# Performance work log

Hardware: AMD Instinct MI355X
Metric: run time of the kernel (lower is better)

Reference implementation:

```python
import jax, jax.numpy as jnp
import numpy as np

N = 40000            # atoms
ER = 2_500_000       # radial edges
EA = 1_200_000       # angular edges
P = 4_000_000        # angle triples
NUM_SPECIES = 4      # H,C,N,O
CUTOFF = 5.2
ANG_CUTOFF = 3.5
RADIAL_ETA = 16.0
ANGULAR_ETA = 8.0
RDIV = 16
ADIV = 4
ZETA = 32.0
ASEC = 4
RSTART = 0.8
ASTART = 0.8


def setup_inputs() -> dict:
    key = jax.random.key(0)
    ks = jax.random.split(key, 12)
    species = jax.random.randint(ks[0], (N,), 0, NUM_SPECIES, dtype=jnp.int32)
    rad_distances = jax.random.uniform(ks[1], (ER,), jnp.float32, RSTART, CUTOFF)
    rad_switch = jax.random.uniform(ks[2], (ER,), jnp.float32)
    edge_src = jax.random.randint(ks[3], (ER,), 0, N, dtype=jnp.int32)
    edge_dst = jax.random.randint(ks[4], (ER,), 0, N, dtype=jnp.int32)
    ang_distances = jax.random.uniform(ks[5], (EA,), jnp.float32, ASTART, ANG_CUTOFF)
    ang_switch = jax.random.uniform(ks[6], (EA,), jnp.float32)
    angles = jax.random.uniform(ks[7], (P,), jnp.float32, 0.0, float(np.pi))
    central_atom = jax.random.randint(ks[8], (P,), 0, N, dtype=jnp.int32)
    angle_src = jax.random.randint(ks[9], (P,), 0, EA, dtype=jnp.int32)
    angle_dst = jax.random.randint(ks[10], (P,), 0, EA, dtype=jnp.int32)
    ang_edge_dst = jax.random.randint(ks[11], (EA,), 0, N, dtype=jnp.int32)
    return {
        "species": species,
        "rad_distances": rad_distances,
        "rad_switch": rad_switch,
        "edge_src": edge_src,
        "edge_dst": edge_dst,
        "ang_distances": ang_distances,
        "ang_switch": ang_switch,
        "angles": angles,
        "central_atom": central_atom,
        "angle_src": angle_src,
        "angle_dst": angle_dst,
        "ang_edge_dst": ang_edge_dst,
    }


def _triu_table(nsp):
    s1, s2 = np.triu_indices(nsp, 0)
    t = np.zeros((nsp, nsp), dtype=np.int32)
    t[s1, s2] = np.arange(s1.shape[0], dtype=np.int32)
    t[s2, s1] = t[s1, s2]
    return jnp.asarray(t)


def reference(species, rad_distances, rad_switch, edge_src, edge_dst,
              ang_distances, ang_switch, angles, central_atom,
              angle_src, angle_dst, ang_edge_dst):
    n_atoms = species.shape[0]
    nsp = NUM_SPECIES
    nsp_pair = nsp * (nsp + 1) // 2
    indices = species  # already species-order indices in [0, nsp)

    # ---- radial AEV ----
    shiftR = jnp.asarray(-np.linspace(RSTART, CUTOFF, RDIV + 1)[None, :-1],
                         dtype=rad_distances.dtype)  # [1, RDIV]
    x2 = RADIAL_ETA * (rad_distances[:, None] + shiftR) ** 2       # [ER, RDIV]
    radial_terms = jnp.exp(-x2) * (0.25 * rad_switch)[:, None]
    radial_index = edge_src * nsp + indices[edge_dst]
    radial_aev = jax.ops.segment_sum(radial_terms, radial_index,
                                     num_segments=nsp * n_atoms)
    radial_aev = radial_aev.reshape(n_atoms, nsp * RDIV)

    # ---- angular AEV ----
    dist = 0.5 * ANGULAR_ETA ** 0.5 * ang_distances                # [EA]
    d12 = (dist[angle_src] + dist[angle_dst])[:, None]             # [P, 1]
    angle_start = np.pi / (2 * ASEC)
    shiftZ = jnp.asarray(-(np.linspace(0, np.pi, ASEC + 1) + angle_start)[None, :-1],
                         dtype=dist.dtype)                          # [1, ASEC]
    shiftA = jnp.asarray(-ANGULAR_ETA ** 0.5 *
                         np.linspace(ASTART, ANG_CUTOFF, ADIV + 1)[None, :-1],
                         dtype=dist.dtype)                          # [1, ADIV]
    sw = ang_switch * (2.0 * 0.5 ** ZETA) ** 0.5                   # [EA]
    f1 = sw[angle_src] * sw[angle_dst]                             # [P]
    factor1 = f1[:, None] * (1 + jnp.cos(angles[:, None] + shiftZ)) ** ZETA  # [P, ASEC]
    factor2 = jnp.exp(-(d12 + shiftA) ** 2)                        # [P, ADIV]
    angular_terms = (factor1[:, None, :] * factor2[:, :, None]).reshape(-1, ASEC * ADIV)

    idx_dest = indices[ang_edge_dst]                               # [EA]
    triu = _triu_table(nsp)
    angular_index = central_atom * nsp_pair + triu[idx_dest[angle_src], idx_dest[angle_dst]]
    angular_aev = jax.ops.segment_sum(angular_terms, angular_index,
                                      num_segments=nsp_pair * n_atoms)
    angular_aev = angular_aev.reshape(n_atoms, nsp_pair * ASEC * ADIV)

    return jnp.concatenate((radial_aev, angular_aev), axis=-1)     # [N, 224]
```

## Files before the change

### kernel.cpp

```cpp
#include <hip/hip_runtime.h>


constexpr int kOutCols  = 224;
constexpr int kAngBase  = 64;
constexpr int kABUCK    = 64;
constexpr int kMaxBins  = 640;
constexpr int kSCap     = 4096;
constexpr int kNBR      = 640;
constexpr int kNBA      = 1024;
constexpr int kRCap     = 4608;
constexpr int kACap     = 7168;
constexpr int kRC       = 12;

__device__ __constant__ int c_triu[16] = {0,1,2,3, 1,4,5,6, 2,5,7,8, 3,6,8,9};
__device__ __constant__ float c_ca[4] = {0.92387953f, 0.38268343f, -0.38268343f, -0.92387953f};
__device__ __constant__ float c_sa[4] = {0.38268343f, 0.92387953f,  0.92387953f,  0.38268343f};
__device__ __constant__ float c_sh[4] = {-2.2627417f, -4.1719303f, -6.0811183f, -7.9903066f};

constexpr float kThQ  = 20860.437f;
constexpr float kRevD = 7.6295109e-6f;
constexpr float kD12B = 2.2627417f;
constexpr float kD12S = 1.4974026e-2f;
constexpr float kF1D  = 1.1732081e-13f;
constexpr float kRdS  = 930.6818f;
constexpr float kRdD  = 1.0744811e-3f;
constexpr float kRswD = 6.1050061e-5f;

__device__ __forceinline__ int scan1024_exc(int cv, int tid, int* wsum, int* total)
{
    int lane = tid & 63, wv = tid >> 6;
    int x = cv;
    #pragma unroll
    for (int o = 1; o < 64; o <<= 1) {
        int t = __shfl_up(x, o, 64);
        if (lane >= o) x += t;
    }
    if (lane == 63) wsum[wv] = x;
    __syncthreads();
    if (wv == 0 && lane < 16) {
        int s = wsum[lane];
        #pragma unroll
        for (int o = 1; o < 16; o <<= 1) {
            int t = __shfl_up(s, o, 64);
            if (lane >= o) s += t;
        }
        wsum[lane] = s;
    }
    __syncthreads();
    int base = (wv == 0) ? 0 : wsum[wv - 1];
    *total = wsum[15];
    return base + x - cv;
}

__global__ void prep(const float* __restrict__ ang_d, const float* __restrict__ ang_sw,
                     const int* __restrict__ aed, const int* __restrict__ species,
                     unsigned short* __restrict__ eaq, int EA)
{
    int i = blockIdx.x * blockDim.x + threadIdx.x;
    if (i >= EA) return;
    float dq = fmaxf(ang_d[i] - 0.8f, 0.0f) * (255.0f / 2.7f);
    unsigned qd = min((unsigned)(dq + 0.5f), 255u);
    unsigned qs = min((unsigned)(fmaxf(ang_sw[i], 0.0f) * 63.0f + 0.5f), 63u);
    unsigned sp = (unsigned)species[aed[i]];
    eaq[i] = (unsigned short)(qd | (qs << 8) | (sp << 14));
}

__global__ __launch_bounds__(1024)
void scat(const float* __restrict__ rd, const float* __restrict__ rsw,
          const int* __restrict__ esrc, const int* __restrict__ edst,
          const int* __restrict__ species,
          unsigned* __restrict__ rrec, int* __restrict__ offRT, int ER, int chR,
          const float* __restrict__ angles, const int* __restrict__ cat,
          const int* __restrict__ asrc, const int* __restrict__ adst,
          const unsigned short* __restrict__ eaq,
          uint2* __restrict__ arec, int* __restrict__ offAT, int P, int chA)
{
    __shared__ uint2 sbuf[kSCap];
    __shared__ int cnt[kMaxBins], off[kMaxBins + 1], cur[kMaxBins];
    __shared__ int wsum[16];
    int tid = threadIdx.x;
    for (int t = tid; t < kMaxBins; t += 1024) cnt[t] = 0;
    __syncthreads();

    if (blockIdx.x < kNBR) {
        int sb  = blockIdx.x;
        int beg = sb * chR, end = min(beg + chR, ER);
        int n   = max(0, end - beg);
        unsigned* rstage = (unsigned*)sbuf;
        unsigned v0 = 0, v1 = 0, v2 = 0, v3 = 0;
        int k0 = 0, k1 = 0, k2 = 0, k3 = 0;
        bool have = false;
        int i0 = beg + tid * 4;
        if (i0 < end) {
            float4 d4 = *reinterpret_cast<const float4*>(rd + i0);
            float4 s4 = *reinterpret_cast<const float4*>(rsw + i0);
            int4   e4 = *reinterpret_cast<const int4*>(esrc + i0);
            int4   t4 = *reinterpret_cast<const int4*>(edst + i0);
            unsigned sa = (unsigned)species[t4.x], sb2 = (unsigned)species[t4.y];
            unsigned sc2 = (unsigned)species[t4.z], sd = (unsigned)species[t4.w];
            auto bld = [](float d, float s, int e, unsigned sp, unsigned& v, int& k) {
                unsigned qd = min((unsigned)(fmaxf(d - 0.8f, 0.0f) * kRdS + 0.5f), 4095u);
                unsigned qs = min((unsigned)(fmaxf(s, 0.0f) * 4095.0f + 0.5f), 4095u);
                v = qd | (qs << 12) | (sp << 24) | ((unsigned)(e & 63) << 26);
                k = e >> 6;
            };
            bld(d4.x, s4.x, e4.x, sa,  v0, k0);
            bld(d4.y, s4.y, e4.y, sb2, v1, k1);
            bld(d4.z, s4.z, e4.z, sc2, v2, k2);
            bld(d4.w, s4.w, e4.w, sd,  v3, k3);
            have = true;
            atomicAdd(&cnt[k0], 1); atomicAdd(&cnt[k1], 1);
            atomicAdd(&cnt[k2], 1); atomicAdd(&cnt[k3], 1);
        }
        __syncthreads();
        int cv = (tid < kMaxBins) ? cnt[tid] : 0;
        int tot;
        int exc = scan1024_exc(cv, tid, wsum, &tot);
        if (tid < kMaxBins) { off[tid] = exc; cur[tid] = exc; }
        if (tid == 0) off[kMaxBins] = tot;
        __syncthreads();
        if (have) {
            rstage[atomicAdd(&cur[k0], 1)] = v0;
            rstage[atomicAdd(&cur[k1], 1)] = v1;
            rstage[atomicAdd(&cur[k2], 1)] = v2;
            rstage[atomicAdd(&cur[k3], 1)] = v3;
        }
        __syncthreads();
        for (int s = tid; s < n; s += 1024) rrec[beg + s] = rstage[s];
        for (int t = tid; t <= kMaxBins; t += 1024) offRT[t * kNBR + sb] = off[t];
    } else {
        int sb  = blockIdx.x - kNBR;
        int beg = sb * chA, end = min(beg + chA, P);
        int n   = max(0, end - beg);
        uint2 r0, r1, r2, r3;
        int k0 = 0, k1 = 0, k2 = 0, k3 = 0;
        bool have = false;
        int i0 = beg + tid * 4;
        if (i0 < end) {
            uint4  s4 = *reinterpret_cast<const uint4*>(asrc + i0);
            uint4  d4 = *reinterpret_cast<const uint4*>(adst + i0);
            float4 t4 = *reinterpret_cast<const float4*>(angles + i0);
            int4   c4 = *reinterpret_cast<const int4*>(cat + i0);
            unsigned qa0 = eaq[s4.x], qb0 = eaq[d4.x];
            unsigned qa1 = eaq[s4.y], qb1 = eaq[d4.y];
            unsigned qa2 = eaq[s4.z], qb2 = eaq[d4.z];
            unsigned qa3 = eaq[s4.w], qb3 = eaq[d4.w];
            auto bld = [](unsigned qa, unsigned qb, float th, int atom, uint2& rv, int& key) {
                unsigned qd12 = (qa & 255u) + (qb & 255u);
                unsigned qf1  = ((qa >> 8) & 63u) * ((qb >> 8) & 63u);
                int pair = c_triu[(qa >> 14) * 4 + (qb >> 14)];
                unsigned qt = min((unsigned)(fmaxf(th, 0.0f) * kThQ + 0.5f), 65535u);
                rv.x = qt | (qd12 << 16);
                rv.y = qf1 | ((unsigned)((atom & 63) * 10 + pair) << 16);
                key = atom >> 6;
            };
            bld(qa0, qb0, t4.x, c4.x, r0, k0);
            bld(qa1, qb1, t4.y, c4.y, r1, k1);
            bld(qa2, qb2, t4.z, c4.z, r2, k2);
            bld(qa3, qb3, t4.w, c4.w, r3, k3);
            have = true;
            atomicAdd(&cnt[k0], 1); atomicAdd(&cnt[k1], 1);
            atomicAdd(&cnt[k2], 1); atomicAdd(&cnt[k3], 1);
        }
        __syncthreads();
        int cv = (tid < kMaxBins) ? cnt[tid] : 0;
        int tot;
        int exc = scan1024_exc(cv, tid, wsum, &tot);
        if (tid < kMaxBins) { off[tid] = exc; cur[tid] = exc; }
        if (tid == 0) off[kMaxBins] = tot;
        __syncthreads();
        if (have) {
            sbuf[atomicAdd(&cur[k0], 1)] = r0;
            sbuf[atomicAdd(&cur[k1], 1)] = r1;
            sbuf[atomicAdd(&cur[k2], 1)] = r2;
            sbuf[atomicAdd(&cur[k3], 1)] = r3;
        }
        __syncthreads();
        for (int s = tid; s < n; s += 1024) arec[beg + s] = sbuf[s];
        for (int t = tid; t <= kMaxBins; t += 1024) offAT[t * kNBA + sb] = off[t];
    }
}

__global__ __launch_bounds__(1024)
void acc_rad(const unsigned* __restrict__ rrec, const int* __restrict__ offRT,
             int chR, float* __restrict__ out, int N)
{
    __shared__ unsigned rb[kRCap];
    __shared__ int cnt[64], off[65], cur[64];
    int b = blockIdx.x, tid = threadIdx.x;
    int gstart = 0, glen = 0;
    if (tid < kNBR) {
        int s0 = offRT[b * kNBR + tid];
        int s1 = offRT[(b + 1) * kNBR + tid];
        gstart = tid * chR + s0;
        glen   = s1 - s0;
    }
    unsigned rr[kRC];
    int gl = min(glen, kRC);
    #pragma unroll
    for (int q = 0; q < kRC; ++q) if (q < gl) rr[q] = rrec[gstart + q];
    if (tid < 64) cnt[tid] = 0;
    __syncthreads();
    #pragma unroll
    for (int q = 0; q < kRC; ++q) if (q < gl) atomicAdd(&cnt[(rr[q] >> 26) & 63], 1);
    for (int p = gstart + kRC; p < gstart + glen; ++p)
        atomicAdd(&cnt[(rrec[p] >> 26) & 63], 1);
    __syncthreads();
    if (tid < 64) {
        int x = cnt[tid], v = x;
        #pragma unroll
        for (int o = 1; o < 64; o <<= 1) {
            int t = __shfl_up(v, o, 64);
            if (tid >= o) v += t;
        }
        off[tid] = v - x; cur[tid] = v - x;
        if (tid == 63) off[64] = v;
    }
    __syncthreads();
    #pragma unroll
    for (int q = 0; q < kRC; ++q)
        if (q < gl) {
            int pos = atomicAdd(&cur[(rr[q] >> 26) & 63], 1);
            if (pos < kRCap) rb[pos] = rr[q];
        }
    for (int p = gstart + kRC; p < gstart + glen; ++p) {
        unsigned r = rrec[p];
        int pos = atomicAdd(&cur[(r >> 26) & 63], 1);
        if (pos < kRCap) rb[pos] = r;
    }
    __syncthreads();
    int lane = tid & 63, wave = tid >> 6;
    int q = lane >> 4, k = lane & 15;
    float ck = fmaf(0.275f, (float)k, 0.8f);
    for (int row = wave; row < kABUCK; row += 16) {
        int s  = min(off[row], kRCap);
        int e1 = min(off[row + 1], kRCap);
        float a0 = 0, a1 = 0, a2 = 0, a3 = 0;
        for (int p = s + q; p < e1; p += 4) {
            unsigned r = rb[p];
            float d  = fmaf((float)(r & 4095u), kRdD, 0.8f);
            float sw = (float)((r >> 12) & 4095u) * kRswD;
            int sp   = (r >> 24) & 3;
            float x  = d - ck;
            float v  = sw * __expf(-16.0f * x * x);
            a0 += (sp == 0) ? v : 0.0f;
            a1 += (sp == 1) ? v : 0.0f;
            a2 += (sp == 2) ? v : 0.0f;
            a3 += (sp == 3) ? v : 0.0f;
        }
        a0 += __shfl_xor(a0, 16, 64); a0 += __shfl_xor(a0, 32, 64);
        a1 += __shfl_xor(a1, 16, 64); a1 += __shfl_xor(a1, 32, 64);
        a2 += __shfl_xor(a2, 16, 64); a2 += __shfl_xor(a2, 32, 64);
        a3 += __shfl_xor(a3, 16, 64); a3 += __shfl_xor(a3, 32, 64);
        float val = (q == 0) ? a0 : (q == 1) ? a1 : (q == 2) ? a2 : a3;
        int atom = b * kABUCK + row;
        if (atom < N) out[(size_t)atom * kOutCols + lane] = val;
    }
}

__global__ __launch_bounds__(1024)
void acc_ang(const uint2* __restrict__ arec, const int* __restrict__ offAT,
             int chA, float* __restrict__ out, int N)
{
    __shared__ uint2 ab[kACap];
    __shared__ int cnt[640], off[641], cur[640];
    __shared__ int wsum[16];
    int b = blockIdx.x, tid = threadIdx.x;
    int s0 = offAT[b * kNBA + tid];
    int s1 = offAT[(b + 1) * kNBA + tid];
    int gstart = tid * chA + s0;
    int glen   = s1 - s0;
    uint2 rr[kRC];
    int gl = min(glen, kRC);
    #pragma unroll
    for (int q = 0; q < kRC; ++q) if (q < gl) rr[q] = arec[gstart + q];
    for (int t = tid; t < 640; t += 1024) cnt[t] = 0;
    __syncthreads();
    #pragma unroll
    for (int q = 0; q < kRC; ++q) if (q < gl) atomicAdd(&cnt[rr[q].y >> 16], 1);
    for (int p = gstart + kRC; p < gstart + glen; ++p)
        atomicAdd(&cnt[arec[p].y >> 16], 1);
    __syncthreads();
    int cv = (tid < 640) ? cnt[tid] : 0;
    int tot;
    int exc = scan1024_exc(cv, tid, wsum, &tot);
    if (tid < 640) { off[tid] = exc; cur[tid] = exc; }
    if (tid == 0) off[640] = tot;
    __syncthreads();
    #pragma unroll
    for (int q = 0; q < kRC; ++q)
        if (q < gl) {
            int pos = atomicAdd(&cur[rr[q].y >> 16], 1);
            if (pos < kACap) ab[pos] = rr[q];
        }
    for (int p = gstart + kRC; p < gstart + glen; ++p) {
        uint2 r = arec[p];
        int pos = atomicAdd(&cur[r.y >> 16], 1);
        if (pos < kACap) ab[pos] = r;
    }
    __syncthreads();
    int g = tid >> 4, lam = tid & 15;
    int q = lam >> 2, j = lam & 3;
    float caj = c_ca[j], saj = c_sa[j];
    int atom = b * kABUCK + g;
    if (atom < N) {
        float* orow = out + (size_t)atom * kOutCols + kAngBase;
        for (int pr = 0; pr < 10; ++pr) {
            int s  = min(off[g * 10 + pr], kACap);
            int e1 = min(off[g * 10 + pr + 1], kACap);
            float s0v = 0, s1v = 0, s2v = 0, s3v = 0;
            for (int p = s + q; p < e1; p += 4) {
                uint2 r = ab[p];
                float rev = (float)(r.x & 0xFFFFu) * kRevD;
                float d12 = fmaf((float)(r.x >> 16), kD12S, kD12B);
                float f1  = (float)(r.y & 0xFFFFu) * kF1D;
                float sn, cs;
                asm("v_sin_f32 %0, %1" : "=v"(sn) : "v"(rev));
                asm("v_cos_f32 %0, %1" : "=v"(cs) : "v"(rev));
                float cj = fmaf(cs, caj, sn * saj);
                float t  = 1.0f + cj;
                float t2 = t * t, t4 = t2 * t2, t8 = t4 * t4, t16 = t8 * t8;
                float w  = f1 * (t16 * t16);
                float x0 = d12 + c_sh[0]; s0v = fmaf(w, __expf(-x0 * x0), s0v);
                float x1 = d12 + c_sh[1]; s1v = fmaf(w, __expf(-x1 * x1), s1v);
                float x2 = d12 + c_sh[2]; s2v = fmaf(w, __expf(-x2 * x2), s2v);
                float x3 = d12 + c_sh[3]; s3v = fmaf(w, __expf(-x3 * x3), s3v);
            }
            s0v += __shfl_xor(s0v, 4, 64); s0v += __shfl_xor(s0v, 8, 64);
            s1v += __shfl_xor(s1v, 4, 64); s1v += __shfl_xor(s1v, 8, 64);
            s2v += __shfl_xor(s2v, 4, 64); s2v += __shfl_xor(s2v, 8, 64);
            s3v += __shfl_xor(s3v, 4, 64); s3v += __shfl_xor(s3v, 8, 64);
            float val = (q == 0) ? s0v : (q == 1) ? s1v : (q == 2) ? s2v : s3v;
            orow[pr * 16 + lam] = val;
        }
    }
}

__global__ void radial_kernel(const float* __restrict__ rd, const float* __restrict__ rsw,
                              const int* __restrict__ esrc, const int* __restrict__ edst,
                              const int* __restrict__ species,
                              float* __restrict__ out, int ER)
{
    int i = blockIdx.x * blockDim.x + threadIdx.x;
    if (i >= ER) return;
    float d   = rd[i];
    float sw  = 0.25f * rsw[i];
    int   src = esrc[i];
    int   sp  = species[edst[i]];
    float* base = out + (size_t)src * kOutCols + sp * 16;
    float t = (d - 0.8f) * (1.0f / 0.275f);
    int klo = max(0, (int)ceilf(t - 4.0f));
    int khi = min(15, (int)floorf(t + 4.0f));
    for (int k = klo; k <= khi; ++k) {
        float x = d - fmaf(0.275f, (float)k, 0.8f);
        float v = sw * __expf(-16.0f * x * x);
        if (v > 1e-8f) unsafeAtomicAdd(base + k, v);
    }
}

__global__ void angular_fallback(const float* __restrict__ angles, const int* __restrict__ cat,
                                 const int* __restrict__ asrc, const int* __restrict__ adst,
                                 const float* __restrict__ ang_d, const float* __restrict__ ang_sw,
                                 const int* __restrict__ aed, const int* __restrict__ species,
                                 float* __restrict__ out, int P)
{
    int i = blockIdx.x * blockDim.x + threadIdx.x;
    if (i >= P) return;
    int e1i = asrc[i], e2i = adst[i];
    float d1 = 1.41421356237f * ang_d[e1i];
    float d2 = 1.41421356237f * ang_d[e2i];
    float w1 = 2.1579187e-05f * ang_sw[e1i];
    float w2 = 2.1579187e-05f * ang_sw[e2i];
    int sp1 = species[aed[e1i]], sp2 = species[aed[e2i]];
    float d12 = d1 + d2;
    float f1  = w1 * w2;
    int pair = c_triu[sp1 * 4 + sp2];
    float* base = out + (size_t)cat[i] * kOutCols + kAngBase + pair * 16;

    float s, c;
    __sincosf(angles[i], &s, &c);
    const float ca0 = 0.92387953f, sa0 = 0.38268343f;
    float cth[4];
    cth[0] = fmaf(c,  ca0, s * sa0);
    cth[1] = fmaf(c,  sa0, s * ca0);
    cth[2] = fmaf(c, -sa0, s * ca0);
    cth[3] = fmaf(c, -ca0, s * sa0);
    float fac1[4];
    #pragma unroll
    for (int j = 0; j < 4; ++j) {
        float t  = 1.0f + cth[j];
        float t2 = t * t, t4 = t2 * t2, t8 = t4 * t4, t16 = t8 * t8;
        fac1[j]  = f1 * (t16 * t16);
    }
    const float shiftA[4] = {-2.2627417f, -4.1719303f, -6.0811183f, -7.9903066f};
    #pragma unroll
    for (int ii = 0; ii < 4; ++ii) {
        float x  = d12 + shiftA[ii];
        float f2 = __expf(-x * x);
        if (f2 < 1e-7f) continue;
        #pragma unroll
        for (int j = 0; j < 4; ++j) {
            float v = f2 * fac1[j];
            if (v > 1e-8f) unsafeAtomicAdd(base + ii * 4 + j, v);
        }
    }
}

extern "C" void kernel_launch(void* const* d_in, const int* in_sizes, int n_in,
                              void* d_out, int out_size, void* d_ws, size_t ws_size,
                              hipStream_t stream)
{
    const int*   species = (const int*)  d_in[0];
    const float* rad_d   = (const float*)d_in[1];
    const float* rad_sw  = (const float*)d_in[2];
    const int*   esrc    = (const int*)  d_in[3];
    const int*   edst    = (const int*)  d_in[4];
    const float* ang_d   = (const float*)d_in[5];
    const float* ang_sw  = (const float*)d_in[6];
    const float* angles  = (const float*)d_in[7];
    const int*   cat     = (const int*)  d_in[8];
    const int*   asrc    = (const int*)  d_in[9];
    const int*   adst    = (const int*)  d_in[10];
    const int*   aed     = (const int*)  d_in[11];
    float* out = (float*)d_out;

    const int N  = in_sizes[0];
    const int ER = in_sizes[1];
    const int EA = in_sizes[5];
    const int P  = in_sizes[7];

    const int NB  = (N + kABUCK - 1) / kABUCK;
    const int chR = (((ER + kNBR - 1) / kNBR) + 3) & ~3;
    const int chA = (((P  + kNBA - 1) / kNBA) + 3) & ~3;

    char* w = (char*)d_ws;
    size_t pos = 0;
    auto take = [&](size_t nbytes) {
        size_t cur = pos;
        pos = (pos + nbytes + 255) & ~(size_t)255;
        return cur;
    };
    size_t ea_o   = take((size_t)EA * 2);
    size_t rrec_o = take((size_t)kNBR * chR * 4);
    size_t arec_o = take((size_t)kNBA * chA * 8);
    size_t ort_o  = take((size_t)(kMaxBins + 1) * kNBR * 4);
    size_t oat_o  = take((size_t)(kMaxBins + 1) * kNBA * 4);
    const size_t need = pos;

    const bool sorted_ok = (ws_size >= need) && (NB <= kMaxBins) &&
                           (chR <= kSCap) && (chA <= kSCap) &&
                           ((P & 3) == 0) && ((ER & 3) == 0);

    if (sorted_ok) {
        unsigned short* eaq = (unsigned short*)(w + ea_o);
        unsigned* rrec  = (unsigned*)(w + rrec_o);
        uint2*    arec  = (uint2*)(w + arec_o);
        int*      offRT = (int*)(w + ort_o);
        int*      offAT = (int*)(w + oat_o);

        prep<<<(EA + 255) / 256, 256, 0, stream>>>(ang_d, ang_sw, aed, species, eaq, EA);
        scat<<<kNBR + kNBA, 1024, 0, stream>>>(rad_d, rad_sw, esrc, edst, species,
                                               rrec, offRT, ER, chR,
                                               angles, cat, asrc, adst, eaq,
                                               arec, offAT, P, chA);
        acc_rad<<<NB, 1024, 0, stream>>>(rrec, offRT, chR, out, N);
        acc_ang<<<NB, 1024, 0, stream>>>(arec, offAT, chA, out, N);
    } else {
        hipMemsetAsync(d_out, 0, (size_t)out_size * sizeof(float), stream);
        radial_kernel<<<(ER + 255) / 256, 256, 0, stream>>>(rad_d, rad_sw, esrc, edst, species, out, ER);
        angular_fallback<<<(P + 255) / 256, 256, 0, stream>>>(angles, cat, asrc, adst,
                                                              ang_d, ang_sw, aed, species, out, P);
    }
}
```

Before: 176.7 us.

## Replace count-then-scatter with single-pass fixed-capacity bin staging in scat

The scatter kernel no longer counts bin sizes in one pass and then scatters in a second pass with separate atomics. Each record is atomically inserted once into a fixed-capacity per-bin slot region in shared memory, and any record beyond a bin's capacity goes to a small overflow buffer. After the prefix scan, records are written out to their global sorted positions from the slots and the overflow list. This removes one barrier and one round of shared atomics per element, at the cost of a larger shared footprint (about 61 KB for sbuf plus 8 KB for the overflow buffer), a sparse strided write-out loop, and silent loss of records if overflow exceeds 512.

New measurement: 178.7 us. Within noise of the previous version (+1.1%).

```diff
diff --git a/kernel.cpp b/kernel.cpp
--- a/kernel.cpp
+++ b/kernel.cpp
@@ -11,6 +11,9 @@
 constexpr int kRCap     = 4608;
 constexpr int kACap     = 7168;
 constexpr int kRC       = 12;
+constexpr int kCapR     = 16;
+constexpr int kCapA     = 12;
+constexpr int kOvf      = 512;
 
 __device__ __constant__ int c_triu[16] = {0,1,2,3, 1,4,5,6, 2,5,7,8, 3,6,8,9};
 __device__ __constant__ float c_ca[4] = {0.92387953f, 0.38268343f, -0.38268343f, -0.92387953f};
@@ -75,21 +78,20 @@
           const unsigned short* __restrict__ eaq,
           uint2* __restrict__ arec, int* __restrict__ offAT, int P, int chA)
 {
-    __shared__ uint2 sbuf[kSCap];
-    __shared__ int cnt[kMaxBins], off[kMaxBins + 1], cur[kMaxBins];
+    __shared__ uint2 sbuf[kMaxBins * kCapA];
+    __shared__ int cur[kMaxBins], off[kMaxBins + 1];
     __shared__ int wsum[16];
+    __shared__ int ovfn;
+    __shared__ uint4 ovfb[kOvf];
     int tid = threadIdx.x;
-    for (int t = tid; t < kMaxBins; t += 1024) cnt[t] = 0;
-    __syncthreads();
 
     if (blockIdx.x < kNBR) {
+        unsigned* stage = (unsigned*)sbuf;
+        for (int t = tid; t < kMaxBins; t += 1024) cur[t] = t * kCapR;
+        if (tid == 0) ovfn = 0;
+        __syncthreads();
         int sb  = blockIdx.x;
         int beg = sb * chR, end = min(beg + chR, ER);
-        int n   = max(0, end - beg);
-        unsigned* rstage = (unsigned*)sbuf;
-        unsigned v0 = 0, v1 = 0, v2 = 0, v3 = 0;
-        int k0 = 0, k1 = 0, k2 = 0, k3 = 0;
-        bool have = false;
         int i0 = beg + tid * 4;
         if (i0 < end) {
             float4 d4 = *reinterpret_cast<const float4*>(rd + i0);
@@ -104,37 +106,46 @@
                 v = qd | (qs << 12) | (sp << 24) | ((unsigned)(e & 63) << 26);
                 k = e >> 6;
             };
+            unsigned v0, v1, v2, v3; int k0, k1, k2, k3;
             bld(d4.x, s4.x, e4.x, sa,  v0, k0);
             bld(d4.y, s4.y, e4.y, sb2, v1, k1);
             bld(d4.z, s4.z, e4.z, sc2, v2, k2);
             bld(d4.w, s4.w, e4.w, sd,  v3, k3);
-            have = true;
-            atomicAdd(&cnt[k0], 1); atomicAdd(&cnt[k1], 1);
-            atomicAdd(&cnt[k2], 1); atomicAdd(&cnt[k3], 1);
-        }
-        __syncthreads();
-        int cv = (tid < kMaxBins) ? cnt[tid] : 0;
+            auto ins = [&](int k, unsigned v) {
+                int pos = atomicAdd(&cur[k], 1);
+                int loc = pos - k * kCapR;
+                if (loc < kCapR) stage[pos] = v;
+                else {
+                    int o = atomicAdd(&ovfn, 1);
+                    if (o < kOvf) { ovfb[o].x = (unsigned)k; ovfb[o].y = (unsigned)loc; ovfb[o].z = v; }
+                }
+            };
+            ins(k0, v0); ins(k1, v1); ins(k2, v2); ins(k3, v3);
+        }
+        __syncthreads();
+        int cv = (tid < kMaxBins) ? (cur[tid] - tid * kCapR) : 0;
         int tot;
         int exc = scan1024_exc(cv, tid, wsum, &tot);
-        if (tid < kMaxBins) { off[tid] = exc; cur[tid] = exc; }
+        if (tid < kMaxBins) off[tid] = exc;
         if (tid == 0) off[kMaxBins] = tot;
-        __syncthreads();
-        if (have) {
-            rstage[atomicAdd(&cur[k0], 1)] = v0;
-            rstage[atomicAdd(&cur[k1], 1)] = v1;
-            rstage[atomicAdd(&cur[k2], 1)] = v2;
-            rstage[atomicAdd(&cur[k3], 1)] = v3;
-        }
-        __syncthreads();
-        for (int s = tid; s < n; s += 1024) rrec[beg + s] = rstage[s];
+        if (tid < kMaxBins) cur[tid] = min(cv, kCapR);
+        __syncthreads();
+        for (int s = tid; s < kMaxBins * kCapR; s += 1024) {
+            int bin = s >> 4, loc = s & (kCapR - 1);
+            if (loc < cur[bin]) rrec[beg + off[bin] + loc] = stage[s];
+        }
+        int no = min(ovfn, kOvf);
+        for (int o = tid; o < no; o += 1024) {
+            uint4 e = ovfb[o];
+            rrec[beg + off[e.x] + (int)e.y] = e.z;
+        }
         for (int t = tid; t <= kMaxBins; t += 1024) offRT[t * kNBR + sb] = off[t];
     } else {
+        for (int t = tid; t < kMaxBins; t += 1024) cur[t] = t * kCapA;
+        if (tid == 0) ovfn = 0;
+        __syncthreads();
         int sb  = blockIdx.x - kNBR;
         int beg = sb * chA, end = min(beg + chA, P);
-        int n   = max(0, end - beg);
-        uint2 r0, r1, r2, r3;
-        int k0 = 0, k1 = 0, k2 = 0, k3 = 0;
-        bool have = false;
         int i0 = beg + tid * 4;
         if (i0 < end) {
             uint4  s4 = *reinterpret_cast<const uint4*>(asrc + i0);
@@ -154,29 +165,40 @@
                 rv.y = qf1 | ((unsigned)((atom & 63) * 10 + pair) << 16);
                 key = atom >> 6;
             };
+            uint2 r0, r1, r2, r3; int k0, k1, k2, k3;
             bld(qa0, qb0, t4.x, c4.x, r0, k0);
             bld(qa1, qb1, t4.y, c4.y, r1, k1);
             bld(qa2, qb2, t4.z, c4.z, r2, k2);
             bld(qa3, qb3, t4.w, c4.w, r3, k3);
-            have = true;
-            atomicAdd(&cnt[k0], 1); atomicAdd(&cnt[k1], 1);
-            atomicAdd(&cnt[k2], 1); atomicAdd(&cnt[k3], 1);
-        }
-        __syncthreads();
-        int cv = (tid < kMaxBins) ? cnt[tid] : 0;
+            auto ins = [&](int k, uint2 r) {
+                int pos = atomicAdd(&cur[k], 1);
+                int loc = pos - k * kCapA;
+                if (loc < kCapA) sbuf[pos] = r;
+                else {
+                    int o = atomicAdd(&ovfn, 1);
+                    if (o < kOvf) { ovfb[o].x = (unsigned)k; ovfb[o].y = (unsigned)loc; ovfb[o].z = r.x; ovfb[o].w = r.y; }
+                }
+            };
+            ins(k0, r0); ins(k1, r1); ins(k2, r2); ins(k3, r3);
+        }
+        __syncthreads();
+        int cv = (tid < kMaxBins) ? (cur[tid] - tid * kCapA) : 0;
         int tot;
         int exc = scan1024_exc(cv, tid, wsum, &tot);
-        if (tid < kMaxBins) { off[tid] = exc; cur[tid] = exc; }
+        if (tid < kMaxBins) off[tid] = exc;
         if (tid == 0) off[kMaxBins] = tot;
-        __syncthreads();
-        if (have) {
-            sbuf[atomicAdd(&cur[k0], 1)] = r0;
-            sbuf[atomicAdd(&cur[k1], 1)] = r1;
-            sbuf[atomicAdd(&cur[k2], 1)] = r2;
-            sbuf[atomicAdd(&cur[k3], 1)] = r3;
-        }
-        __syncthreads();
-        for (int s = tid; s < n; s += 1024) arec[beg + s] = sbuf[s];
+        if (tid < kMaxBins) cur[tid] = min(cv, kCapA);
+        __syncthreads();
+        for (int s = tid; s < kMaxBins * kCapA; s += 1024) {
+            int bin = s / kCapA, loc = s - bin * kCapA;
+            if (loc < cur[bin]) arec[beg + off[bin] + loc] = sbuf[s];
+        }
+        int no = min(ovfn, kOvf);
+        for (int o = tid; o < no; o += 1024) {
+            uint4 e = ovfb[o];
+            uint2 r; r.x = e.z; r.y = e.w;
+            arec[beg + off[e.x] + (int)e.y] = r;
+        }
         for (int t = tid; t <= kMaxBins; t += 1024) offAT[t * kNBA + sb] = off[t];
     }
 }
```
